# Kernel tuning notes

Measured on AMD Instinct MI355X. Metric: run time of the kernel, lower is better.

The kernel has to match this reference:

```python
import jax, jax.numpy as jnp
import numpy as np

N = 50000      # n_nodes
E = 800000     # directed edges (symmetric set, no self-loops)
D_IN = 128
D_HID = 128
EPS = 1e-5     # LayerNorm eps (torch default)


def setup_inputs() -> dict:
    rng = np.random.default_rng(0)
    a = rng.integers(0, N, 700000, dtype=np.int64)
    b = rng.integers(0, N, 700000, dtype=np.int64)
    m = a != b
    a, b = a[m], b[m]
    # symmetric, deduplicated edge set (no self-loops); shuffle before truncation
    keys = np.unique(np.concatenate([a * N + b, b * N + a]))
    keys = rng.permutation(keys)[:E]
    row = (keys // N).astype(np.int32)
    col = (keys % N).astype(np.int32)
    ks = jax.random.split(jax.random.key(0), 6)
    return {
        "x": jax.random.normal(ks[0], (N, D_IN), jnp.float32),
        "W0": jax.random.normal(ks[1], (D_IN, D_HID), jnp.float32) / np.float32(np.sqrt(D_IN)),
        "b0": jnp.zeros((D_HID,), jnp.float32),
        "W1": jax.random.normal(ks[2], (D_HID, D_HID), jnp.float32) / np.float32(np.sqrt(D_HID)),
        "b1": jnp.zeros((D_HID,), jnp.float32),
        "ln1_g": jnp.ones((D_HID,), jnp.float32),
        "ln1_b": jnp.zeros((D_HID,), jnp.float32),
        "ln2_g": jnp.ones((D_HID,), jnp.float32),
        "ln2_b": jnp.zeros((D_HID,), jnp.float32),
        "drop_W": jax.random.normal(ks[3], (1, 2), jnp.float32) * 10.0,
        "drop_b": jnp.zeros((1,), jnp.float32),
        "row": jnp.asarray(row),
        "col": jnp.asarray(col),
    }


def _layernorm(h, g, b):
    mu = jnp.mean(h, axis=-1, keepdims=True)
    var = jnp.var(h, axis=-1, keepdims=True)
    return (h - mu) * jax.lax.rsqrt(var + EPS) * g + b


def _att_coef(h, row, col, drop_W, drop_b):
    # fused on-device version of the CPU att_coef: per-edge cosine sim,
    # threshold, row-l1-normalize, learned binary drop, self-loop lam, exp.
    n = h.shape[0]
    norms = jnp.sqrt(jnp.sum(h * h, axis=1))                      # [n]
    sim = jnp.sum(h[row] * h[col], axis=1) / (norms[row] * norms[col])  # [E]
    sim = jnp.where(sim < 0.1, 0.0, sim)
    rs = jax.ops.segment_sum(sim, row, num_segments=n)            # row l1 norms
    att = sim / jnp.where(rs[row] > 0, rs[row], 1.0)
    # reverse-edge lookup att[col,row] via sorted uint32 keys (n*n < 2**32)
    nn = jnp.uint32(n)
    keys = row.astype(jnp.uint32) * nn + col.astype(jnp.uint32)
    order = jnp.argsort(keys)
    sk = keys[order]
    rk = col.astype(jnp.uint32) * nn + row.astype(jnp.uint32)
    pos = jnp.clip(jnp.searchsorted(sk, rk), 0, keys.shape[0] - 1)
    att_rev = jnp.where(sk[pos] == rk, att[order[pos]], 0.0)
    # drop_learn: Linear(2,1) -> sigmoid -> Threshold(0.5,0) -> Threshold(-0.49,1)
    # net effect: binary mask = 1 if sigmoid(score) > 0.5 else 0
    score = jax.nn.sigmoid(att * drop_W[0, 0] + att_rev * drop_W[0, 1] + drop_b[0])
    att = att * (score > 0.5).astype(h.dtype)
    deg = jax.ops.segment_sum((att != 0).astype(h.dtype), row, num_segments=n)
    lam = 1.0 / (deg + 1.0)                                       # self-loop weight
    w_e = jnp.where(att != 0, jnp.exp(att), 0.0)                  # exp only on stored nnz
    w_diag = jnp.exp(lam)
    # original computes attention on CPU numpy -> detached from autograd
    return jax.lax.stop_gradient(w_e), jax.lax.stop_gradient(w_diag)


def _conv(h, w_e, w_diag, row, col, W, b):
    s = h @ W                                                      # [n, d_out]
    agg = jax.ops.segment_sum(w_e[:, None] * s[col], row, num_segments=h.shape[0])
    return agg + w_diag[:, None] * s + b


def reference(x, W0, b0, W1, b1, ln1_g, ln1_b, ln2_g, ln2_b, drop_W, drop_b, row, col):
    h = x
    # layer 0
    w_e, w_d = _att_coef(h, row, col, drop_W, drop_b)
    h = _conv(h, w_e, w_d, row, col, W0, b0)
    h = jax.nn.relu(_layernorm(h, ln1_g, ln1_b))   # dropout: eval mode -> identity
    # layer 1
    w_e, w_d = _att_coef(h, row, col, drop_W, drop_b)
    h = _conv(h, w_e, w_d, row, col, W1, b1)
    h = jax.nn.relu(_layernorm(h, ln2_g, ln2_b))
    # final block: source bug reuses the last loop conv (convs[-2] == W1,b1)
    w_e, w_d = _att_coef(h, row, col, drop_W, drop_b)
    h = _conv(h, w_e, w_d, row, col, W1, b1)
    return jax.nn.log_softmax(h, axis=-1)
```

## Files before the change

kernel.cpp:

```cpp
#include <hip/hip_runtime.h>
#include <hip/hip_bf16.h>

#define D 128
#define EPS 1e-5f
#define SCAP 32
#define GB 10

__global__ __launch_bounds__(256) void k_pre(
    const int* __restrict__ row, int* __restrict__ cnt, int E,
    const float* __restrict__ h, float* __restrict__ nrm, int N, int cB) {
  if ((int)blockIdx.x < cB) {
    int e = blockIdx.x * 256 + threadIdx.x;
    if (e < E) atomicAdd(&cnt[row[e]], 1);
  } else {
    int i = (blockIdx.x - cB) * 8 + (threadIdx.x >> 5);
    int sub = threadIdx.x & 31;
    if (i >= N) return;
    float4 a = ((const float4*)(h + (size_t)i * D))[sub];
    float v = a.x * a.x + a.y * a.y + a.z * a.z + a.w * a.w;
    for (int off = 16; off > 0; off >>= 1) v += __shfl_down(v, off, 32);
    if (sub == 0) nrm[i] = sqrtf(v);
  }
}

__global__ __launch_bounds__(256) void k_bsum(const int* __restrict__ cnt,
                                              int* __restrict__ bsum) {
  int t = threadIdx.x;
  int base = blockIdx.x * 1024 + t * 4;
  int4 c4 = ((const int4*)(cnt + base))[0];
  int s = c4.x + c4.y + c4.z + c4.w;
  for (int off = 32; off > 0; off >>= 1) s += __shfl_down(s, off);
  __shared__ int sh[4];
  if ((t & 63) == 0) sh[t >> 6] = s;
  __syncthreads();
  if (t == 0) bsum[blockIdx.x] = sh[0] + sh[1] + sh[2] + sh[3];
}

__global__ __launch_bounds__(256) void k_bscan(const int* __restrict__ bsum,
                                               int* __restrict__ boff, int nb,
                                               int* __restrict__ rptr, int N, int E) {
  __shared__ int sh[256];
  int t = threadIdx.x;
  int v = (t < nb) ? bsum[t] : 0;
  sh[t] = v;
  __syncthreads();
  for (int off = 1; off < 256; off <<= 1) {
    int u = (t >= off) ? sh[t - off] : 0;
    __syncthreads();
    sh[t] += u;
    __syncthreads();
  }
  if (t < nb) boff[t] = sh[t] - v;
  if (t == 0) rptr[N] = E;
}

__global__ __launch_bounds__(256) void k_apply(const int* __restrict__ cnt,
                                               const int* __restrict__ boff,
                                               int* __restrict__ rptr, int N) {
  __shared__ int sh[256];
  int t = threadIdx.x;
  int base = blockIdx.x * 1024 + t * 4;
  int4 c4 = ((const int4*)(cnt + base))[0];
  int e1 = c4.x, e2 = c4.x + c4.y, e3 = c4.x + c4.y + c4.z;
  int tot = e3 + c4.w;
  sh[t] = tot;
  __syncthreads();
  for (int off = 1; off < 256; off <<= 1) {
    int u = (t >= off) ? sh[t - off] : 0;
    __syncthreads();
    sh[t] += u;
    __syncthreads();
  }
  int o = sh[t] - tot + boff[blockIdx.x];
  if (base + 0 < N) rptr[base + 0] = o;
  if (base + 1 < N) rptr[base + 1] = o + e1;
  if (base + 2 < N) rptr[base + 2] = o + e2;
  if (base + 3 < N) rptr[base + 3] = o + e3;
}

__global__ __launch_bounds__(256) void k_scatter(
    const int* __restrict__ row, const int* __restrict__ col,
    const int* __restrict__ rptr, int* __restrict__ cur,
    int* __restrict__ colS, int E) {
  int e = blockIdx.x * 256 + threadIdx.x;
  if (e < E) {
    int r = row[e];
    int p = rptr[r] + atomicAdd(&cur[r], 1);
    colS[p] = col[e];
  }
}

__global__ __launch_bounds__(256) void k_rev(const int* __restrict__ colS,
                                             const int* __restrict__ rptr,
                                             int* __restrict__ rev, int N) {
  int grp = threadIdx.x >> 5, sub = threadIdx.x & 31;
  int i = blockIdx.x * 8 + grp;
  if (i >= N) return;
  int p0 = rptr[i], p1 = rptr[i + 1];
  for (int p = p0 + sub; p < p1; p += 32) {
    int c = colS[p];
    int q1 = rptr[c + 1];
    int rv = -1;
    for (int q = rptr[c]; q < q1; ++q)
      if (colS[q] == i) { rv = q; break; }
    rev[p] = rv;
  }
}

__global__ __launch_bounds__(256) void k_sim(
    const float* __restrict__ h, const float* __restrict__ nrm,
    const int* __restrict__ rptr, const int* __restrict__ colS,
    const int* __restrict__ rev, float* __restrict__ simS, int N) {
  __shared__ int cL[8 * SCAP];
  __shared__ int pL[8 * SCAP];
  __shared__ int rL[8 * SCAP];
  __shared__ float nL[8 * SCAP];
  int grp = threadIdx.x >> 5;
  int sub = threadIdx.x & 31;
  int half = grp & 1;
  int i = blockIdx.x * 8 + grp;
  if (i >= N) return;
  int gb = grp * SCAP;
  int p0 = rptr[i], p1 = rptr[i + 1];
  float4 ai = ((const float4*)(h + (size_t)i * D))[sub];
  float ni = nrm[i];
  for (int base = p0; base < p1; base += SCAP) {
    int p = base + sub;
    bool inr = p < p1;
    int c = inr ? colS[p] : 0;
    int rv = inr ? rev[p] : 0;
    bool ok = inr && (c > i || rv < 0);
    unsigned long long mb = __ballot(ok);
    unsigned mh = (unsigned)(mb >> (half * 32));
    int pos = __popc(mh & ((1u << sub) - 1u));
    int K = __popc(mh);
    if (ok) {
      cL[gb + pos] = c;
      pL[gb + pos] = p;
      rL[gb + pos] = rv;
      nL[gb + pos] = nrm[c];
    }
    __builtin_amdgcn_wave_barrier();
    for (int j0 = 0; j0 < K; j0 += GB) {
      int cc_[GB];
      bool vv[GB];
      float4 b[GB];
#pragma unroll
      for (int k = 0; k < GB; ++k) {
        int idx = j0 + k;
        vv[k] = idx < K;
        cc_[k] = vv[k] ? cL[gb + idx] : i;
      }
#pragma unroll
      for (int k = 0; k < GB; ++k)
        b[k] = ((const float4*)(h + (size_t)cc_[k] * D))[sub];
#pragma unroll
      for (int k = 0; k < GB; ++k) {
        float v = ai.x * b[k].x + ai.y * b[k].y + ai.z * b[k].z + ai.w * b[k].w;
        for (int off = 16; off > 0; off >>= 1) v += __shfl_down(v, off, 32);
        if (sub == 0 && vv[k]) {
          int idx = j0 + k;
          float sm = v / (ni * nL[gb + idx]);
          sm = (sm < 0.1f) ? 0.0f : sm;
          simS[pL[gb + idx]] = sm;
          int rv2 = rL[gb + idx];
          if (rv2 >= 0) simS[rv2] = sm;
        }
      }
    }
    __builtin_amdgcn_wave_barrier();
  }
}

__global__ __launch_bounds__(256) void k_rs(const float* __restrict__ simS,
                                            const int* __restrict__ rptr,
                                            float* __restrict__ rsE, int N) {
  int i = blockIdx.x * 256 + threadIdx.x;
  if (i >= N) return;
  int p1 = rptr[i + 1];
  float rs = 0.f;
  for (int p = rptr[i]; p < p1; ++p) rs += simS[p];
  rsE[i] = (rs > 0.f) ? rs : 1.f;
}

__global__ __launch_bounds__(256) void k_gemm(const float* __restrict__ h,
                                              const float* __restrict__ W,
                                              float* __restrict__ S, int N) {
  __shared__ float Ws[64 * D];
  int t = threadIdx.x;
  int i0 = blockIdx.x * 64;
  int tx = t & 15, ty = t >> 4;
  int gi[4];
  bool vld[4];
#pragma unroll
  for (int r = 0; r < 4; ++r) {
    gi[r] = i0 + ty * 4 + r;
    vld[r] = gi[r] < N;
  }
  float acc[4][8] = {};
  for (int ph = 0; ph < 2; ++ph) {
    __syncthreads();
    for (int ch = 0; ch < 8; ++ch) {
      int q = t + 256 * ch;
      ((float4*)Ws)[q] = ((const float4*)(W + (size_t)ph * 64 * D))[q];
    }
    __syncthreads();
    for (int kk = 0; kk < 16; ++kk) {
      float4 a4[4];
#pragma unroll
      for (int r = 0; r < 4; ++r)
        a4[r] = vld[r] ? ((const float4*)(h + (size_t)gi[r] * D))[ph * 16 + kk]
                       : make_float4(0.f, 0.f, 0.f, 0.f);
      float4 b0[4], b1[4];
#pragma unroll
      for (int k = 0; k < 4; ++k) {
        b0[k] = ((const float4*)(Ws + (kk * 4 + k) * D))[tx];
        b1[k] = ((const float4*)(Ws + (kk * 4 + k) * D))[16 + tx];
      }
#pragma unroll
      for (int r = 0; r < 4; ++r) {
        float4 a = a4[r];
#pragma unroll
        for (int c = 0; c < 4; ++c) {
          acc[r][c] += a.x * (&b0[0].x)[c] + a.y * (&b0[1].x)[c] +
                       a.z * (&b0[2].x)[c] + a.w * (&b0[3].x)[c];
          acc[r][4 + c] += a.x * (&b1[0].x)[c] + a.y * (&b1[1].x)[c] +
                           a.z * (&b1[2].x)[c] + a.w * (&b1[3].x)[c];
        }
      }
    }
  }
#pragma unroll
  for (int r = 0; r < 4; ++r) {
    if (vld[r]) {
      ((float4*)(S + (size_t)gi[r] * D))[tx] =
          make_float4(acc[r][0], acc[r][1], acc[r][2], acc[r][3]);
      ((float4*)(S + (size_t)gi[r] * D))[16 + tx] =
          make_float4(acc[r][4], acc[r][5], acc[r][6], acc[r][7]);
    }
  }
}

template <int MODE>
__global__ __launch_bounds__(256) void k_combine(
    const float* __restrict__ s, const float* __restrict__ simS,
    const float* __restrict__ rsE, const int* __restrict__ rev,
    const int* __restrict__ rptr, const int* __restrict__ colS,
    const float* __restrict__ bias, const float* __restrict__ g,
    const float* __restrict__ be, const float* __restrict__ dWp,
    const float* __restrict__ dbp, float* __restrict__ outF,
    float* __restrict__ nrmOut, int N) {
  __shared__ float wL[8 * 32];
  __shared__ int cLd[8 * 32];
  int grp = threadIdx.x >> 5, sub = threadIdx.x & 31;
  int half = grp & 1;
  int i = blockIdx.x * 8 + grp;
  if (i >= N) return;
  int gb = grp * 32;
  float w0 = dWp[0], w1 = dWp[1], bd = dbp[0];
  int p0 = rptr[i], p1 = rptr[i + 1];
  float ri = rsE[i];
  float4 acc = make_float4(0.f, 0.f, 0.f, 0.f);
  int deg = 0;
  for (int base = p0; base < p1; base += 32) {
    int p = base + sub;
    bool inr = p < p1;
    float sm = inr ? simS[p] : 0.f;
    int c = inr ? colS[p] : 0;
    int rv = inr ? rev[p] : -1;
    bool keep = false;
    float a = 0.f;
    if (sm != 0.f) {
      a = sm / ri;
      float ar = (rv >= 0) ? sm / rsE[c] : 0.f;
      float x = a * w0 + ar * w1 + bd;
      float sc = (x >= 0.f) ? 1.f / (1.f + expf(-x)) : expf(x) / (1.f + expf(x));
      keep = sc > 0.5f;
    }
    unsigned long long mb = __ballot(keep);
    unsigned mh = (unsigned)(mb >> (half * 32));
    int pos = __popc(mh & ((1u << sub) - 1u));
    int K = __popc(mh);
    if (keep) {
      wL[gb + pos] = expf(a);
      cLd[gb + pos] = c;
    }
    __builtin_amdgcn_wave_barrier();
    deg += K;
    for (int j0 = 0; j0 < K; j0 += 8) {
      int cc_[8];
      float ww[8];
      float4 b[8];
#pragma unroll
      for (int k = 0; k < 8; ++k) {
        int idx = j0 + k;
        bool vv = idx < K;
        cc_[k] = vv ? cLd[gb + idx] : i;
        ww[k] = vv ? wL[gb + idx] : 0.f;
      }
#pragma unroll
      for (int k = 0; k < 8; ++k)
        b[k] = ((const float4*)(s + (size_t)cc_[k] * D))[sub];
#pragma unroll
      for (int k = 0; k < 8; ++k) {
        acc.x += ww[k] * b[k].x; acc.y += ww[k] * b[k].y;
        acc.z += ww[k] * b[k].z; acc.w += ww[k] * b[k].w;
      }
    }
    __builtin_amdgcn_wave_barrier();
  }
  float wd = expf(1.0f / (float)(deg + 1));
  float4 sv = ((const float4*)(s + (size_t)i * D))[sub];
  float4 bb = ((const float4*)bias)[sub];
  float4 v = make_float4(acc.x + wd * sv.x + bb.x, acc.y + wd * sv.y + bb.y,
                         acc.z + wd * sv.z + bb.z, acc.w + wd * sv.w + bb.w);
  if (MODE == 0) {
    float sm = v.x + v.y + v.z + v.w;
    for (int off = 16; off > 0; off >>= 1) sm += __shfl_down(sm, off, 32);
    float mu = __shfl(sm, 0, 32) * (1.f / 128.f);
    float4 dv = make_float4(v.x - mu, v.y - mu, v.z - mu, v.w - mu);
    float q = dv.x * dv.x + dv.y * dv.y + dv.z * dv.z + dv.w * dv.w;
    for (int off = 16; off > 0; off >>= 1) q += __shfl_down(q, off, 32);
    float var = __shfl(q, 0, 32) * (1.f / 128.f);
    float rstd = rsqrtf(var + EPS);
    float4 gg = ((const float4*)g)[sub];
    float4 eb = ((const float4*)be)[sub];
    float4 y = make_float4(fmaxf(dv.x * rstd * gg.x + eb.x, 0.f),
                           fmaxf(dv.y * rstd * gg.y + eb.y, 0.f),
                           fmaxf(dv.z * rstd * gg.z + eb.z, 0.f),
                           fmaxf(dv.w * rstd * gg.w + eb.w, 0.f));
    ((float4*)(outF + (size_t)i * D))[sub] = y;
    float q2 = y.x * y.x + y.y * y.y + y.z * y.z + y.w * y.w;
    for (int off = 16; off > 0; off >>= 1) q2 += __shfl_down(q2, off, 32);
    if (sub == 0) nrmOut[i] = sqrtf(q2);
  } else {
    float mx = fmaxf(fmaxf(v.x, v.y), fmaxf(v.z, v.w));
    for (int off = 16; off > 0; off >>= 1) mx = fmaxf(mx, __shfl_down(mx, off, 32));
    float m = __shfl(mx, 0, 32);
    float es = expf(v.x - m) + expf(v.y - m) + expf(v.z - m) + expf(v.w - m);
    for (int off = 16; off > 0; off >>= 1) es += __shfl_down(es, off, 32);
    float l = logf(__shfl(es, 0, 32)) + m;
    ((float4*)(outF + (size_t)i * D))[sub] =
        make_float4(v.x - l, v.y - l, v.z - l, v.w - l);
  }
}

extern "C" void kernel_launch(void* const* d_in, const int* in_sizes, int n_in,
                              void* d_out, int out_size, void* d_ws, size_t ws_size,
                              hipStream_t stream) {
  const float* x   = (const float*)d_in[0];
  const float* W0  = (const float*)d_in[1];
  const float* b0  = (const float*)d_in[2];
  const float* W1  = (const float*)d_in[3];
  const float* b1  = (const float*)d_in[4];
  const float* g1  = (const float*)d_in[5];
  const float* be1 = (const float*)d_in[6];
  const float* g2  = (const float*)d_in[7];
  const float* be2 = (const float*)d_in[8];
  const float* dW  = (const float*)d_in[9];
  const float* db  = (const float*)d_in[10];
  const int* row   = (const int*)d_in[11];
  const int* col   = (const int*)d_in[12];
  int N = in_sizes[0] / D;
  int E = in_sizes[11];
  float* out = (float*)d_out;

  float* base = (float*)d_ws;
  size_t off = 0;
  auto alloc = [&](size_t elems) {
    float* p = base + off;
    off += (elems + 3) & ~(size_t)3;
    return p;
  };
  size_t N128 = (size_t)N * D;
  int nb = (N + 1023) / 1024;
  int NpadS = nb * 1024;
  float* hA   = alloc(N128);
  float* hB   = alloc(N128);
  float* s    = alloc(N128);
  int*   colS = (int*)alloc(E);
  int*   rev  = (int*)alloc(E);
  float* simS = alloc(E);
  int*   cc   = (int*)alloc((size_t)2 * NpadS);
  int*   cnt  = cc;
  int*   cur  = cc + NpadS;
  int*   rptr = (int*)alloc(N + 1);
  float* rsE  = alloc(N);
  float* nrm  = alloc(N);
  int*   bsum = (int*)alloc(nb);
  int*   boff = (int*)alloc(nb);
  (void)ws_size; (void)n_in; (void)out_size;

  int cB = (E + 255) / 256;
  int nB = (N + 7) / 8;
  int nG = (N + 63) / 64;
  int nSim = (N + 7) / 8;
  int nRs = (N + 255) / 256;
  int nC = (N + 7) / 8;

  hipMemsetAsync(cc, 0, (size_t)2 * NpadS * sizeof(int), stream);
  k_pre<<<cB + nB, 256, 0, stream>>>(row, cnt, E, x, nrm, N, cB);
  k_bsum<<<nb, 256, 0, stream>>>(cnt, bsum);
  k_bscan<<<1, 256, 0, stream>>>(bsum, boff, nb, rptr, N, E);
  k_apply<<<nb, 256, 0, stream>>>(cnt, boff, rptr, N);
  k_scatter<<<cB, 256, 0, stream>>>(row, col, rptr, cur, colS, E);
  k_rev<<<nSim, 256, 0, stream>>>(colS, rptr, rev, N);

  auto layer = [&](const float* hin, float* hout, const float* Wf,
                   const float* bf, const float* gf, const float* bef,
                   float* nrmOut, int mode) {
    k_sim<<<nSim, 256, 0, stream>>>(hin, nrm, rptr, colS, rev, simS, N);
    k_rs<<<nRs, 256, 0, stream>>>(simS, rptr, rsE, N);
    k_gemm<<<nG, 256, 0, stream>>>(hin, Wf, s, N);
    if (mode == 0)
      k_combine<0><<<nC, 256, 0, stream>>>(s, simS, rsE, rev, rptr, colS, bf, gf,
                                           bef, dW, db, hout, nrmOut, N);
    else
      k_combine<1><<<nC, 256, 0, stream>>>(s, simS, rsE, rev, rptr, colS, bf, gf,
                                           bef, dW, db, hout, nullptr, N);
  };
  layer(x, hA, W0, b0, g1, be1, nrm, 0);
  layer(hA, hB, W1, b1, g2, be2, nrm, 0);
  layer(hB, out, W1, b1, nullptr, nullptr, nullptr, 1);
}
```

Before: 608.9 us.

## Replace CSR scatter with two-pass bucketed scatter using LDS atomics

The single-pass edge scatter, which issued one global atomic per edge into a per-row cursor and wrote colS at random positions, is replaced by two passes. The first pass groups edges into 128-row buckets, packing the local row and column into one word, with the bucket cursors padded to avoid contention. The second pass sorts each bucket into exact row positions using shared-memory atomics, so colS writes stay local. This trades an extra pass over a packed intermediate array for fewer scattered global atomics and better write locality. The packing limits column indices to 25 bits, and bcur relies on the padded region being large enough for 16-int spacing.

```diff
diff --git a/kernel.cpp b/kernel.cpp
--- a/kernel.cpp
+++ b/kernel.cpp
@@ -78,15 +78,35 @@
   if (base + 3 < N) rptr[base + 3] = o + e3;
 }
 
-__global__ __launch_bounds__(256) void k_scatter(
+__global__ __launch_bounds__(256) void k_bktA(
     const int* __restrict__ row, const int* __restrict__ col,
-    const int* __restrict__ rptr, int* __restrict__ cur,
-    int* __restrict__ colS, int E) {
+    const int* __restrict__ rptr, int* __restrict__ bcur,
+    unsigned* __restrict__ pairs, int E) {
   int e = blockIdx.x * 256 + threadIdx.x;
   if (e < E) {
     int r = row[e];
-    int p = rptr[r] + atomicAdd(&cur[r], 1);
-    colS[p] = col[e];
+    int b = r >> 7;
+    int q = rptr[b << 7] + atomicAdd(&bcur[b * 16], 1);
+    pairs[q] = ((unsigned)(r & 127) << 25) | (unsigned)col[e];
+  }
+}
+
+__global__ __launch_bounds__(256) void k_bktB(
+    const unsigned* __restrict__ pairs, const int* __restrict__ rptr,
+    int* __restrict__ colS, int N) {
+  __shared__ int curL[128];
+  int b = blockIdx.x;
+  int r0 = b << 7;
+  int rend = min(r0 + 128, N);
+  int q0 = rptr[r0], q1 = rptr[rend];
+  if (threadIdx.x < 128) curL[threadIdx.x] = 0;
+  __syncthreads();
+  for (int q = q0 + threadIdx.x; q < q1; q += 256) {
+    unsigned pk = pairs[q];
+    int lr = pk >> 25;
+    int c = (int)(pk & 0x1FFFFFFu);
+    int p = rptr[r0 + lr] + atomicAdd(&curL[lr], 1);
+    colS[p] = c;
   }
 }
 
@@ -381,9 +401,10 @@
   int*   colS = (int*)alloc(E);
   int*   rev  = (int*)alloc(E);
   float* simS = alloc(E);
+  unsigned* pairs = (unsigned*)alloc(E);
   int*   cc   = (int*)alloc((size_t)2 * NpadS);
   int*   cnt  = cc;
-  int*   cur  = cc + NpadS;
+  int*   bcur = cc + NpadS;
   int*   rptr = (int*)alloc(N + 1);
   float* rsE  = alloc(N);
   float* nrm  = alloc(N);
@@ -397,13 +418,15 @@
   int nSim = (N + 7) / 8;
   int nRs = (N + 255) / 256;
   int nC = (N + 7) / 8;
+  int NBKT = (N + 127) / 128;
 
   hipMemsetAsync(cc, 0, (size_t)2 * NpadS * sizeof(int), stream);
   k_pre<<<cB + nB, 256, 0, stream>>>(row, cnt, E, x, nrm, N, cB);
   k_bsum<<<nb, 256, 0, stream>>>(cnt, bsum);
   k_bscan<<<1, 256, 0, stream>>>(bsum, boff, nb, rptr, N, E);
   k_apply<<<nb, 256, 0, stream>>>(cnt, boff, rptr, N);
-  k_scatter<<<cB, 256, 0, stream>>>(row, col, rptr, cur, colS, E);
+  k_bktA<<<cB, 256, 0, stream>>>(row, col, rptr, bcur, pairs, E);
+  k_bktB<<<NBKT, 256, 0, stream>>>(pairs, rptr, colS, N);
   k_rev<<<nSim, 256, 0, stream>>>(colS, rptr, rev, N);
 
   auto layer = [&](const float* hin, float* hout, const float* Wf,
```

Result: no change. 612.5 us (+0.6%).
